# Optimization experiments

Hardware: AMD Instinct MI355X
Metric: run time of the kernel (lower is better)

## Reference

```python
import jax, jax.numpy as jnp
import numpy as np

B, M, L, IN_C, MID_C, OUT_C = 1, 128, 256, 256, 32, 128


def setup_inputs() -> dict:
    key = jax.random.key(0)
    k_x, k_proj, k_final = jax.random.split(key, 3)
    return {
        "x1d": jax.random.normal(k_x, (B, M, L, IN_C), dtype=jnp.float32),
        "norm_w": jnp.ones((IN_C,), dtype=jnp.float32),
        "norm_b": jnp.zeros((IN_C,), dtype=jnp.float32),
        "proj_w": jax.random.normal(k_proj, (2 * MID_C, IN_C), dtype=jnp.float32) * 0.02,
        "proj_b": jnp.zeros((2 * MID_C,), dtype=jnp.float32),
        "final_w": jax.random.normal(k_final, (OUT_C, MID_C * MID_C), dtype=jnp.float32) * 0.02,
        "final_b": jnp.zeros((OUT_C,), dtype=jnp.float32),
    }


def reference(x1d, norm_w, norm_b, proj_w, proj_b, final_w, final_b):
    # LayerNorm over channel dim
    mu = jnp.mean(x1d, axis=-1, keepdims=True)
    var = jnp.mean(jnp.square(x1d - mu), axis=-1, keepdims=True)
    x = (x1d - mu) * jax.lax.rsqrt(var + 1e-5) * norm_w + norm_b

    mid_c = proj_w.shape[0] // 2
    # Linear -> (b, m, L, 2*mid_c); view (..., mid_c, 2); chunk & squeeze:
    # i = interleaved even channels, j = interleaved odd channels
    p = jnp.einsum('bmlc,dc->bmld', x, proj_w) + proj_b
    p = p.reshape(*p.shape[:-1], mid_c, 2)
    i, j = p[..., 0], p[..., 1]          # each (b, m, L, mid_c)

    m = x1d.shape[1]
    # Outer product mean over the MSA (m) dimension -> (b, L, L, mid_c, mid_c)
    x2d = jnp.einsum('bmix,bmjy->bijxy', i, j) / m

    b, li, lj = x2d.shape[0], x2d.shape[1], x2d.shape[2]
    flat = x2d.reshape(b, li, lj, mid_c * mid_c)
    out = jnp.einsum('bijf,of->bijo', flat, final_w) + final_b
    return out
```

## Files before the change

kernel.cpp:

```cpp
#include <hip/hip_runtime.h>
#include <hip/hip_bf16.h>

#define DEVINL __device__ __forceinline__

typedef float  f32x4_t  __attribute__((ext_vector_type(4)));
typedef float  f32x16_t __attribute__((ext_vector_type(16)));
typedef short  bf16x8_t __attribute__((ext_vector_type(8)));

#define MFMA16(a,b,c) __builtin_amdgcn_mfma_f32_16x16x32_bf16((a),(b),(c),0,0,0)
#define MFMA32(a,b,c) __builtin_amdgcn_mfma_f32_32x32x16_bf16((a),(b),(c),0,0,0)

DEVINL unsigned short f2bf(float f) {
  union { float f; unsigned u; } v; v.f = f;
  unsigned r = v.u + 0x7fffu + ((v.u >> 16) & 1u);
  return (unsigned short)(r >> 16);
}

DEVINL unsigned pk2bf(float lo, float hi) {
  union { __hip_bfloat162 h2; unsigned u; } v;
  v.h2 = __float22bfloat162_rn(make_float2(lo, hi));
  return v.u;
}


__global__ __launch_bounds__(256) void kA(const float* __restrict__ x,
                                          const float* __restrict__ nw,
                                          const float* __restrict__ nb,
                                          const float* __restrict__ pw,
                                          const float* __restrict__ pb,
                                          const float* __restrict__ fw,
                                          unsigned short* __restrict__ Wb,
                                          unsigned short* __restrict__ Ig,
                                          unsigned short* __restrict__ Jg) {
  if (blockIdx.x >= 1024) {
    int i = (blockIdx.x - 1024) * 256 + threadIdx.x;
    float4 v = ((const float4*)fw)[i];
    int o  = i >> 8;
    int f0 = (i & 255) * 4;
    ushort4 u;
    u.x = f2bf(v.x); u.y = f2bf(v.y); u.z = f2bf(v.z); u.w = f2bf(v.w);
    size_t off = (size_t)((o >> 5) * 64 + (f0 >> 4)) * 512 + (o & 31) * 16 + ((f0 >> 3) & 1) * 8 + (f0 & 7);
    *(ushort4*)&Wb[off] = u;
    return;
  }
  __shared__ unsigned short xnl[32 * 264];
  __shared__ unsigned short pwl[64 * 264];
  __shared__ unsigned short ep[64 * 36];
  const int tid  = threadIdx.x;
  const int wv   = tid >> 6;
  const int lane = tid & 63;
  const int q    = lane >> 4;
  const int ln16 = lane & 15;
  const int l    = blockIdx.x & 255;
  const int m0   = (blockIdx.x >> 8) * 32;

  const float4* xs = (const float4*)x;
  float4 v[8];
#pragma unroll
  for (int i = 0; i < 8; i++) {
    int row = m0 + i * 4 + wv;
    v[i] = xs[row * 16384 + l * 64 + lane];
  }
  float4 nw4 = ((const float4*)nw)[lane];
  float4 nb4 = ((const float4*)nb)[lane];

#pragma unroll
  for (int i = 0; i < 8; i++) {
    float s  = v[i].x + v[i].y + v[i].z + v[i].w;
    float ss = v[i].x * v[i].x + v[i].y * v[i].y + v[i].z * v[i].z + v[i].w * v[i].w;
#pragma unroll
    for (int off = 32; off > 0; off >>= 1) {
      s  += __shfl_xor(s, off);
      ss += __shfl_xor(ss, off);
    }
    float mu  = s * (1.0f / 256.0f);
    float var = ss * (1.0f / 256.0f) - mu * mu;
    float rs  = rsqrtf(var + 1e-5f);
    ushort4 u;
    u.x = f2bf((v[i].x - mu) * rs * nw4.x + nb4.x);
    u.y = f2bf((v[i].y - mu) * rs * nw4.y + nb4.y);
    u.z = f2bf((v[i].z - mu) * rs * nw4.z + nb4.z);
    u.w = f2bf((v[i].w - mu) * rs * nw4.w + nb4.w);
    *(ushort4*)&xnl[(i * 4 + wv) * 264 + lane * 4] = u;
  }

  const float4* ps = (const float4*)pw;
#pragma unroll
  for (int i = 0; i < 16; i++) {
    float4 w4 = ps[i * 256 + tid];
    ushort4 u;
    u.x = f2bf(w4.x); u.y = f2bf(w4.y); u.z = f2bf(w4.z); u.w = f2bf(w4.w);
    *(ushort4*)&pwl[(i * 4 + wv) * 264 + lane * 4] = u;
  }
  __syncthreads();

  const int rt = wv & 1;
  const int db = (wv >> 1) * 32;
  f32x4_t acc[2] = {{0.f, 0.f, 0.f, 0.f}, {0.f, 0.f, 0.f, 0.f}};
#pragma unroll
  for (int kc = 0; kc < 8; kc++) {
    bf16x8_t a  = *(const bf16x8_t*)&xnl[(rt * 16 + ln16) * 264 + kc * 32 + q * 8];
    bf16x8_t b0 = *(const bf16x8_t*)&pwl[(db + ln16) * 264 + kc * 32 + q * 8];
    bf16x8_t b1 = *(const bf16x8_t*)&pwl[(db + 16 + ln16) * 264 + kc * 32 + q * 8];
    acc[0] = MFMA16(a, b0, acc[0]);
    acc[1] = MFMA16(a, b1, acc[1]);
  }

#pragma unroll
  for (int t2 = 0; t2 < 2; t2++) {
    int d = db + t2 * 16 + ln16;
    float bias  = pb[d];
    float scale = (d & 1) ? 1.0f : (1.0f / 128.0f);
#pragma unroll
    for (int r = 0; r < 4; r++) {
      int mloc = rt * 16 + q * 4 + r;
      ep[d * 36 + mloc] = f2bf((acc[t2][r] + bias) * scale);
    }
  }
  __syncthreads();

  const int h  = tid >> 3;
  const int m4 = tid & 7;
  const size_t off = (size_t)(l * 8 + (m0 >> 4) + (m4 >> 2)) * 512 + h * 16 + ((m4 >> 1) & 1) * 8 + (m4 & 1) * 4;
  ushort4 vi = *(const ushort4*)&ep[(2 * h) * 36 + m4 * 4];
  *(ushort4*)&Ig[off] = vi;
  ushort4 vj = *(const ushort4*)&ep[(2 * h + 1) * 36 + m4 * 4];
  *(ushort4*)&Jg[off] = vj;
}

__global__ __launch_bounds__(512, 4) void kB(const unsigned short* __restrict__ Ig,
                                             const unsigned short* __restrict__ Jg,
                                             const unsigned short* __restrict__ Wb,
                                             const float* __restrict__ fb,
                                             float* __restrict__ out) {
  extern __shared__ unsigned short fl[];
  const int tid  = threadIdx.x;
  const int w    = tid >> 6;
  const int lane = tid & 63;
  const int ln32 = lane & 31;
  const int h    = lane >> 5;
  const int p    = blockIdx.x >> 4;
  const int t2   = blockIdx.x & 15;

  bf16x8_t af[2][8];
#pragma unroll
  for (int il = 0; il < 2; il++)
#pragma unroll
    for (int mc = 0; mc < 8; mc++)
      af[il][mc] = *(const bf16x8_t*)&Ig[(size_t)((p * 2 + il) * 8 + mc) * 512 + ln32 * 16 + h * 8];

  const unsigned short* Jbase = Jg + (size_t)(t2 * 16 + w * 2) * 4096 + ln32 * 16 + h * 8;
  const int eo = ln32 & 7;
  const int oc = ln32 >> 3;

  bf16x8_t bf[2][8];
#pragma unroll
  for (int mc = 0; mc < 8; mc++) bf[0][mc] = *(const bf16x8_t*)&Jbase[mc * 512];

#pragma unroll
  for (int s = 0; s < 2; s++) {
    if (s == 0) {
#pragma unroll
      for (int mc = 0; mc < 8; mc++)
        bf[1][mc] = *(const bf16x8_t*)&Jbase[4096 + mc * 512];
    }
    f32x16_t a0, a1;
#pragma unroll
    for (int i = 0; i < 16; i++) { a0[i] = 0.f; a1[i] = 0.f; }
#pragma unroll
    for (int mc = 0; mc < 8; mc++) {
      a0 = MFMA32(af[0][mc], bf[s][mc], a0);
      a1 = MFMA32(af[1][mc], bf[s][mc], a1);
    }
    const int fr = w * 2 + s;
    unsigned short* fr0 = &fl[fr * 1032 + eo];
    unsigned short* fr1 = &fl[(16 + fr) * 1032 + eo];
#pragma unroll
    for (int rp = 0; rp < 8; rp++) {
      int x0  = (2 * rp & 3) + 8 * (rp >> 1) + 4 * h;
      int cp0 = ((x0 * 4 + oc) ^ (((x0 >> 2) & 3) * 5)) * 8;
      int cp1 = (((x0 + 1) * 4 + oc) ^ ((((x0 + 1) >> 2) & 3) * 5)) * 8;
      unsigned u0 = pk2bf(a0[2 * rp], a0[2 * rp + 1]);
      fr0[cp0] = (unsigned short)u0;
      fr0[cp1] = (unsigned short)(u0 >> 16);
      unsigned u1 = pk2bf(a1[2 * rp], a1[2 * rp + 1]);
      fr1[cp0] = (unsigned short)u1;
      fr1[cp1] = (unsigned short)(u1 >> 16);
    }
  }

  const int ot = w & 3;
  const int kh = w >> 2;
  const unsigned short* Wp = Wb + (size_t)(ot * 64 + kh * 32) * 512 + ln32 * 16 + h * 8;
  bf16x8_t bq[4];
  bq[0] = *(const bf16x8_t*)&Wp[0];
  bq[1] = *(const bf16x8_t*)&Wp[512];

  __syncthreads();

  bq[2] = *(const bf16x8_t*)&Wp[2 * 512];
  bq[3] = *(const bf16x8_t*)&Wp[3 * 512];

  const unsigned short* flp = fl + ln32 * 1032;
#define LDA(kc) (*(const bf16x8_t*)&flp[((((kc) >> 1) * 4 + ((kc) & 1) * 2 + h) ^ ((((kc) >> 3) & 3) * 5)) * 8])

  f32x16_t oa;
#pragma unroll
  for (int i = 0; i < 16; i++) oa[i] = 0.f;

  bf16x8_t a0 = LDA(kh * 32), a1 = LDA(kh * 32 + 1);
#pragma unroll
  for (int c = 0; c < 32; c++) {
    bf16x8_t acur = a0;
    bf16x8_t bcur = bq[c & 3];
    if (c < 31) a0 = a1;
    if (c < 30) a1 = LDA(kh * 32 + c + 2);
    if (c < 28) bq[c & 3] = *(const bf16x8_t*)&Wp[(c + 4) * 512];
    oa = MFMA32(acur, bcur, oa);
  }
#undef LDA

  __syncthreads();
  float* red = (float*)fl;
  if (kh == 1) {
#pragma unroll
    for (int r = 0; r < 16; r++) red[(ot * 16 + r) * 64 + lane] = oa[r];
  }
  __syncthreads();
  if (kh == 0) {
    float bias = fb[ot * 32 + ln32];
    float* op = out + ((size_t)(p * 2) * 256 + t2 * 16) * 128 + ot * 32 + ln32;
#pragma unroll
    for (int r = 0; r < 16; r++) {
      float val = oa[r] + red[(ot * 16 + r) * 64 + lane] + bias;
      int row = (r & 3) + 8 * (r >> 2) + 4 * h;
      op[(row >> 4) * 32768 + (row & 15) * 128] = val;
    }
  }
}

extern "C" void kernel_launch(void* const* d_in, const int* in_sizes, int n_in,
                              void* d_out, int out_size, void* d_ws, size_t ws_size,
                              hipStream_t stream) {
  const float* x1d     = (const float*)d_in[0];
  const float* norm_w  = (const float*)d_in[1];
  const float* norm_b  = (const float*)d_in[2];
  const float* proj_w  = (const float*)d_in[3];
  const float* proj_b  = (const float*)d_in[4];
  const float* final_w = (const float*)d_in[5];
  const float* final_b = (const float*)d_in[6];
  float* outp          = (float*)d_out;

  unsigned short* Wb  = (unsigned short*)d_ws;
  unsigned short* Igp = Wb + 131072;
  unsigned short* Jgp = Igp + 1048576;

  const int kb_lds = 32 * 1032 * 2;
  hipFuncSetAttribute((const void*)kB, hipFuncAttributeMaxDynamicSharedMemorySize, kb_lds);

  kA<<<1152, 256, 0, stream>>>(x1d, norm_w, norm_b, proj_w, proj_b, final_w, Wb, Igp, Jgp);
  kB<<<2048, 512, kb_lds, stream>>>(Igp, Jgp, Wb, final_b, outp);
}
```

Measured before the change: 139.9 us.

## Double kB tile height and transpose final weight feature order

```diff
diff --git a/kernel.cpp b/kernel.cpp
--- a/kernel.cpp
+++ b/kernel.cpp
@@ -33,13 +33,19 @@
                                           unsigned short* __restrict__ Ig,
                                           unsigned short* __restrict__ Jg) {
   if (blockIdx.x >= 1024) {
-    int i = (blockIdx.x - 1024) * 256 + threadIdx.x;
-    float4 v = ((const float4*)fw)[i];
-    int o  = i >> 8;
-    int f0 = (i & 255) * 4;
+    int T = (blockIdx.x - 1024) * 256 + threadIdx.x;
+    int o     = T >> 8;
+    int kpos0 = (T & 255) * 4;
+    int y  = kpos0 >> 5;
+    int x0 = kpos0 & 31;
+    const float* fo = fw + o * 1024 + y;
     ushort4 u;
-    u.x = f2bf(v.x); u.y = f2bf(v.y); u.z = f2bf(v.z); u.w = f2bf(v.w);
-    size_t off = (size_t)((o >> 5) * 64 + (f0 >> 4)) * 512 + (o & 31) * 16 + ((f0 >> 3) & 1) * 8 + (f0 & 7);
+    u.x = f2bf(fo[(x0 + 0) * 32]);
+    u.y = f2bf(fo[(x0 + 1) * 32]);
+    u.z = f2bf(fo[(x0 + 2) * 32]);
+    u.w = f2bf(fo[(x0 + 3) * 32]);
+    size_t off = (size_t)((o >> 5) * 64 + (kpos0 >> 4)) * 512 + (o & 31) * 16
+               + ((kpos0 >> 3) & 1) * 8 + (kpos0 & 7);
     *(ushort4*)&Wb[off] = u;
     return;
   }
@@ -128,64 +134,59 @@
   *(ushort4*)&Jg[off] = vj;
 }
 
-__global__ __launch_bounds__(512, 4) void kB(const unsigned short* __restrict__ Ig,
+__global__ __launch_bounds__(512, 2) void kB(const unsigned short* __restrict__ Ig,
                                              const unsigned short* __restrict__ Jg,
                                              const unsigned short* __restrict__ Wb,
                                              const float* __restrict__ fb,
                                              float* __restrict__ out) {
   extern __shared__ unsigned short fl[];
+  constexpr int P = 1048;
   const int tid  = threadIdx.x;
   const int w    = tid >> 6;
   const int lane = tid & 63;
   const int ln32 = lane & 31;
   const int h    = lane >> 5;
   const int p    = blockIdx.x >> 4;
-  const int t2   = blockIdx.x & 15;
-
-  bf16x8_t af[2][8];
-#pragma unroll
-  for (int il = 0; il < 2; il++)
-#pragma unroll
-    for (int mc = 0; mc < 8; mc++)
-      af[il][mc] = *(const bf16x8_t*)&Ig[(size_t)((p * 2 + il) * 8 + mc) * 512 + ln32 * 16 + h * 8];
-
-  const unsigned short* Jbase = Jg + (size_t)(t2 * 16 + w * 2) * 4096 + ln32 * 16 + h * 8;
-  const int eo = ln32 & 7;
-  const int oc = ln32 >> 3;
-
-  bf16x8_t bf[2][8];
-#pragma unroll
-  for (int mc = 0; mc < 8; mc++) bf[0][mc] = *(const bf16x8_t*)&Jbase[mc * 512];
+  const int t    = blockIdx.x & 15;
+
+  bf16x8_t jb[2][8];
+  const size_t jbase = (size_t)(t * 16 + 2 * w) * 4096 + ln32 * 16 + h * 8;
+#pragma unroll
+  for (int mc = 0; mc < 8; mc++) jb[0][mc] = *(const bf16x8_t*)&Jg[jbase + mc * 512];
+#pragma unroll
+  for (int mc = 0; mc < 8; mc++) jb[1][mc] = *(const bf16x8_t*)&Jg[jbase + 4096 + mc * 512];
 
 #pragma unroll
   for (int s = 0; s < 2; s++) {
-    if (s == 0) {
-#pragma unroll
-      for (int mc = 0; mc < 8; mc++)
-        bf[1][mc] = *(const bf16x8_t*)&Jbase[4096 + mc * 512];
-    }
-    f32x16_t a0, a1;
-#pragma unroll
-    for (int i = 0; i < 16; i++) { a0[i] = 0.f; a1[i] = 0.f; }
-#pragma unroll
-    for (int mc = 0; mc < 8; mc++) {
-      a0 = MFMA32(af[0][mc], bf[s][mc], a0);
-      a1 = MFMA32(af[1][mc], bf[s][mc], a1);
-    }
-    const int fr = w * 2 + s;
-    unsigned short* fr0 = &fl[fr * 1032 + eo];
-    unsigned short* fr1 = &fl[(16 + fr) * 1032 + eo];
-#pragma unroll
-    for (int rp = 0; rp < 8; rp++) {
-      int x0  = (2 * rp & 3) + 8 * (rp >> 1) + 4 * h;
-      int cp0 = ((x0 * 4 + oc) ^ (((x0 >> 2) & 3) * 5)) * 8;
-      int cp1 = (((x0 + 1) * 4 + oc) ^ ((((x0 + 1) >> 2) & 3) * 5)) * 8;
-      unsigned u0 = pk2bf(a0[2 * rp], a0[2 * rp + 1]);
-      fr0[cp0] = (unsigned short)u0;
-      fr0[cp1] = (unsigned short)(u0 >> 16);
-      unsigned u1 = pk2bf(a1[2 * rp], a1[2 * rp + 1]);
-      fr1[cp0] = (unsigned short)u1;
-      fr1[cp1] = (unsigned short)(u1 >> 16);
+    const int jl = 2 * w + s;
+#pragma unroll
+    for (int ilp = 0; ilp < 2; ilp++) {
+      bf16x8_t af[2][8];
+#pragma unroll
+      for (int u = 0; u < 2; u++)
+#pragma unroll
+        for (int mc = 0; mc < 8; mc++)
+          af[u][mc] = *(const bf16x8_t*)&Ig[(size_t)((p * 4 + ilp * 2 + u) * 8 + mc) * 512 + ln32 * 16 + h * 8];
+      f32x16_t c[2];
+#pragma unroll
+      for (int i = 0; i < 16; i++) { c[0][i] = 0.f; c[1][i] = 0.f; }
+#pragma unroll
+      for (int mc = 0; mc < 8; mc++) {
+        c[0] = MFMA32(af[0][mc], jb[s][mc], c[0]);
+        c[1] = MFMA32(af[1][mc], jb[s][mc], c[1]);
+      }
+#pragma unroll
+      for (int u = 0; u < 2; u++) {
+        unsigned short* fr = &fl[((ilp * 2 + u) * 16 + jl) * P];
+#pragma unroll
+        for (int g = 0; g < 4; g++) {
+          int cp = (4 * ln32 + g) ^ (ln32 & 7);
+          uint2 pv;
+          pv.x = pk2bf(c[u][4 * g + 0], c[u][4 * g + 1]);
+          pv.y = pk2bf(c[u][4 * g + 2], c[u][4 * g + 3]);
+          *(uint2*)&fr[cp * 8 + h * 4] = pv;
+        }
+      }
     }
   }
 
@@ -201,22 +202,21 @@
   bq[2] = *(const bf16x8_t*)&Wp[2 * 512];
   bq[3] = *(const bf16x8_t*)&Wp[3 * 512];
 
-  const unsigned short* flp = fl + ln32 * 1032;
-#define LDA(kc) (*(const bf16x8_t*)&flp[((((kc) >> 1) * 4 + ((kc) & 1) * 2 + h) ^ ((((kc) >> 3) & 3) * 5)) * 8])
-
-  f32x16_t oa;
-#pragma unroll
-  for (int i = 0; i < 16; i++) oa[i] = 0.f;
-
-  bf16x8_t a0 = LDA(kh * 32), a1 = LDA(kh * 32 + 1);
-#pragma unroll
-  for (int c = 0; c < 32; c++) {
-    bf16x8_t acur = a0;
-    bf16x8_t bcur = bq[c & 3];
-    if (c < 31) a0 = a1;
-    if (c < 30) a1 = LDA(kh * 32 + c + 2);
-    if (c < 28) bq[c & 3] = *(const bf16x8_t*)&Wp[(c + 4) * 512];
-    oa = MFMA32(acur, bcur, oa);
+#define LDA(rt, kc) (*(const bf16x8_t*)&fl[((rt) * 32 + ln32) * P + \
+    ((((kh * 32 + (kc)) * 2 + h) ^ (((kh * 32 + (kc)) >> 1) & 7)) * 8)])
+
+  f32x16_t o2[2];
+#pragma unroll
+  for (int i = 0; i < 16; i++) { o2[0][i] = 0.f; o2[1][i] = 0.f; }
+
+  bf16x8_t a0 = LDA(0, 0), a1 = LDA(1, 0);
+#pragma unroll
+  for (int kc = 0; kc < 32; kc++) {
+    bf16x8_t ac0 = a0, ac1 = a1, bc = bq[kc & 3];
+    if (kc < 31) { a0 = LDA(0, kc + 1); a1 = LDA(1, kc + 1); }
+    if (kc < 28) bq[kc & 3] = *(const bf16x8_t*)&Wp[(kc + 4) * 512];
+    o2[0] = MFMA32(ac0, bc, o2[0]);
+    o2[1] = MFMA32(ac1, bc, o2[1]);
   }
 #undef LDA
 
@@ -224,17 +224,29 @@
   float* red = (float*)fl;
   if (kh == 1) {
 #pragma unroll
-    for (int r = 0; r < 16; r++) red[(ot * 16 + r) * 64 + lane] = oa[r];
+    for (int rt = 0; rt < 2; rt++) {
+      float* bb = red + (ot * 2 + rt) * 1024 + lane * 2;
+#pragma unroll
+      for (int k = 0; k < 8; k++)
+        *(float2*)&bb[k * 128] = make_float2(o2[rt][2 * k], o2[rt][2 * k + 1]);
+    }
   }
   __syncthreads();
   if (kh == 0) {
-    float bias = fb[ot * 32 + ln32];
-    float* op = out + ((size_t)(p * 2) * 256 + t2 * 16) * 128 + ot * 32 + ln32;
-#pragma unroll
-    for (int r = 0; r < 16; r++) {
-      float val = oa[r] + red[(ot * 16 + r) * 64 + lane] + bias;
-      int row = (r & 3) + 8 * (r >> 2) + 4 * h;
-      op[(row >> 4) * 32768 + (row & 15) * 128] = val;
+    const float bias = fb[ot * 32 + ln32];
+    float* ob = out + ((size_t)(p * 4) * 256 + t * 16) * 128 + ot * 32 + ln32;
+#pragma unroll
+    for (int rt = 0; rt < 2; rt++) {
+      const float* bb = red + (ot * 2 + rt) * 1024 + lane * 2;
+#pragma unroll
+      for (int k = 0; k < 8; k++) {
+        float2 rv = *(const float2*)&bb[k * 128];
+        int r0 = 2 * k, r1 = 2 * k + 1;
+        int br0 = rt * 32 + (r0 & 3) + 8 * (r0 >> 2) + 4 * h;
+        int br1 = rt * 32 + (r1 & 3) + 8 * (r1 >> 2) + 4 * h;
+        ob[(br0 >> 4) * 32768 + (br0 & 15) * 128] = o2[rt][r0] + rv.x + bias;
+        ob[(br1 >> 4) * 32768 + (br1 & 15) * 128] = o2[rt][r1] + rv.y + bias;
+      }
     }
   }
 }
@@ -255,9 +267,9 @@
   unsigned short* Igp = Wb + 131072;
   unsigned short* Jgp = Igp + 1048576;
 
-  const int kb_lds = 32 * 1032 * 2;
+  const int kb_lds = 64 * 1048 * 2;
   hipFuncSetAttribute((const void*)kB, hipFuncAttributeMaxDynamicSharedMemorySize, kb_lds);
 
   kA<<<1152, 256, 0, stream>>>(x1d, norm_w, norm_b, proj_w, proj_b, final_w, Wb, Igp, Jgp);
-  kB<<<2048, 512, kb_lds, stream>>>(Igp, Jgp, Wb, final_b, outp);
-}
+  kB<<<1024, 512, kb_lds, stream>>>(Igp, Jgp, Wb, final_b, outp);
+}
```

Measured after the change: 136.8 us. 1.02x faster.
